# Kernel tuning notes

Hardware: AMD Instinct MI355X
Metric: run time of the kernel (lower is better)

## Reference

```python
import jax, jax.numpy as jnp
import numpy as np

SEQ_LEN = 4096
DIM_HALF = 2048  # x last dim = 2 * DIM_HALF
DIM_OUT = 1024
LN_EPS = 1e-5


def setup_inputs() -> dict:
    key = jax.random.key(0)
    k1, k2, k3 = jax.random.split(key, 3)
    x = jax.random.normal(k1, (SEQ_LEN, 2 * DIM_HALF), dtype=jnp.float32)
    ln_scale = jnp.ones((DIM_HALF,), dtype=jnp.float32)
    # original init is uniform(-eps/n, eps/n); scale randn similarly small
    spatial_weights = jax.random.normal(k2, (SEQ_LEN, SEQ_LEN), dtype=jnp.float32) * (0.001 / SEQ_LEN)
    spatial_biases = jnp.ones((SEQ_LEN, 1), dtype=jnp.float32)
    proj_w = jax.random.normal(k3, (DIM_HALF, DIM_OUT), dtype=jnp.float32) * (1.0 / np.sqrt(DIM_HALF))
    proj_b = jnp.zeros((DIM_OUT,), dtype=jnp.float32)
    return {"x": x, "ln_scale": ln_scale, "spatial_weights": spatial_weights,
            "spatial_biases": spatial_biases, "proj_w": proj_w, "proj_b": proj_b}


def reference(x, ln_scale, spatial_weights, spatial_biases, proj_w, proj_b):
    # split into value half and gate half
    xh, gate = jnp.split(x, 2, axis=-1)  # each (n, d)
    # LayerNorm (scale only, no offset), haiku default eps=1e-5
    mean = jnp.mean(gate, axis=-1, keepdims=True)
    var = jnp.var(gate, axis=-1, keepdims=True)
    gate = (gate - mean) * jax.lax.rsqrt(var + LN_EPS) * ln_scale
    # causal (lower-triangular) masked spatial mixing: out[m,d] = sum_n w[m,n] * gate[n,d]
    n = spatial_weights.shape[0]
    w = jnp.tril(spatial_weights)
    gate = jnp.einsum('nd,mn->md', gate, w) + spatial_biases  # (n, d)
    # gating multiply + output projection
    out = (xh * gate) @ proj_w + proj_b  # (n, dim_out)
    return out
```

## Files before the change

### kernel.cpp

```cpp
#include <hip/hip_runtime.h>
#include <cstdint>
#include <cstddef>

#define SEQ 4096
#define DH 2048
#define DOUT 1024

typedef float f32x4 __attribute__((ext_vector_type(4)));
typedef __bf16 bf16x8 __attribute__((ext_vector_type(8)));


__device__ __forceinline__ unsigned short f2bf(float f) {
  unsigned int u = __float_as_uint(f);
  unsigned int r = (u + 0x7FFFu + ((u >> 16) & 1u)) >> 16;
  return (unsigned short)r;
}

__device__ __forceinline__ void g2l16(const unsigned short* g, unsigned short* l) {
  __builtin_amdgcn_global_load_lds((__attribute__((address_space(1))) void*)(void*)g,
                                   (__attribute__((address_space(3))) void*)l, 16, 0, 0);
}


__global__ __launch_bounds__(256) void ln_stats(const float* __restrict__ x,
                                                float* __restrict__ mv,
                                                float* __restrict__ rv) {
  int row = blockIdx.x;
  const float4* g4 = (const float4*)(x + (size_t)row * (2 * DH) + DH);
  float4 a = g4[threadIdx.x];
  float4 b = g4[threadIdx.x + 256];
  float s  = a.x + a.y + a.z + a.w + b.x + b.y + b.z + b.w;
  float s2 = a.x * a.x + a.y * a.y + a.z * a.z + a.w * a.w +
             b.x * b.x + b.y * b.y + b.z * b.z + b.w * b.w;
#pragma unroll
  for (int o = 32; o > 0; o >>= 1) {
    s  += __shfl_down(s, o);
    s2 += __shfl_down(s2, o);
  }
  __shared__ float red[8];
  int wave = threadIdx.x >> 6;
  if ((threadIdx.x & 63) == 0) { red[wave] = s; red[wave + 4] = s2; }
  __syncthreads();
  if (threadIdx.x == 0) {
    float S  = red[0] + red[1] + red[2] + red[3];
    float S2 = red[4] + red[5] + red[6] + red[7];
    float mean = S * (1.0f / DH);
    float var  = S2 * (1.0f / DH) - mean * mean;
    mv[row] = mean;
    rv[row] = rsqrtf(var + 1e-5f);
  }
}


__global__ __launch_bounds__(256) void norm_tr(const float* __restrict__ x,
                                               const float* __restrict__ mv,
                                               const float* __restrict__ rv,
                                               const float* __restrict__ lns,
                                               unsigned short* __restrict__ gateT) {
  __shared__ float tile[64][65];
  int d0 = blockIdx.x * 64;
  int n0 = blockIdx.y * 64;
#pragma unroll
  for (int i = 0; i < 16; i++) {
    int idx = threadIdx.x + i * 256;
    int r = idx >> 6, c = idx & 63;
    float v = x[(size_t)(n0 + r) * (2 * DH) + DH + d0 + c];
    tile[r][c] = (v - mv[n0 + r]) * rv[n0 + r];
  }
  __syncthreads();
#pragma unroll
  for (int i = 0; i < 16; i++) {
    int idx = threadIdx.x + i * 256;
    int dr = idx >> 6, nc = idx & 63;
    float v = tile[nc][dr] * lns[d0 + dr];
    gateT[(size_t)(d0 + dr) * SEQ + n0 + nc] = f2bf(v);
  }
}


__global__ __launch_bounds__(256) void cast_w_tril(const float* __restrict__ w,
                                                   unsigned short* __restrict__ wb) {
  size_t e = ((size_t)blockIdx.x * 256 + threadIdx.x) * 8;
  int m = (int)(e >> 12);
  int k = (int)(e & 4095);
  uint4 o;
  if (k + 7 <= m) {
    const float4* s = (const float4*)(w + e);
    float4 a = s[0], b = s[1];
    o.x = (unsigned)f2bf(a.x) | ((unsigned)f2bf(a.y) << 16);
    o.y = (unsigned)f2bf(a.z) | ((unsigned)f2bf(a.w) << 16);
    o.z = (unsigned)f2bf(b.x) | ((unsigned)f2bf(b.y) << 16);
    o.w = (unsigned)f2bf(b.z) | ((unsigned)f2bf(b.w) << 16);
  } else if (k > m) {
    o.x = o.y = o.z = o.w = 0u;
  } else {
    unsigned short t[8];
#pragma unroll
    for (int j = 0; j < 8; j++) t[j] = (k + j <= m) ? f2bf(w[e + j]) : (unsigned short)0;
    o.x = (unsigned)t[0] | ((unsigned)t[1] << 16);
    o.y = (unsigned)t[2] | ((unsigned)t[3] << 16);
    o.z = (unsigned)t[4] | ((unsigned)t[5] << 16);
    o.w = (unsigned)t[6] | ((unsigned)t[7] << 16);
  }
  *(uint4*)(wb + e) = o;
}


__global__ __launch_bounds__(256) void proj_tr(const float* __restrict__ pw,
                                               unsigned short* __restrict__ pT) {
  __shared__ float tile[64][65];
  int j0 = blockIdx.x * 64;
  int d0 = blockIdx.y * 64;
#pragma unroll
  for (int i = 0; i < 16; i++) {
    int idx = threadIdx.x + i * 256;
    int r = idx >> 6, c = idx & 63;
    tile[r][c] = pw[(size_t)(d0 + r) * DOUT + j0 + c];
  }
  __syncthreads();
#pragma unroll
  for (int i = 0; i < 16; i++) {
    int idx = threadIdx.x + i * 256;
    int jr = idx >> 6, dc = idx & 63;
    pT[(size_t)(j0 + jr) * DH + d0 + dc] = f2bf(tile[dc][jr]);
  }
}


template <bool PAIR, int EPI>
__global__ __launch_bounds__(256) void gemm12864(const unsigned short* __restrict__ A,
                                                 const unsigned short* __restrict__ BT,
                                                 const float* __restrict__ xfull,
                                                 const float* __restrict__ rbias,
                                                 unsigned short* __restrict__ Pout,
                                                 const float* __restrict__ cbias,
                                                 float* __restrict__ out,
                                                 int N, int K) {
  constexpr int BK = 64;
  __shared__ unsigned short sA[128 * BK];
  __shared__ unsigned short sB[64 * BK];

  const int tid = threadIdx.x;
  const int lane = tid & 63, wave = tid >> 6;
  const int quad = lane >> 4, l16 = lane & 15;
  const int wm = wave >> 1, wn = wave & 1;
  const int bn0 = blockIdx.x * 64;
  const int p = blockIdx.y;

  int sOff[4], sDst[4];
#pragma unroll
  for (int r = 0; r < 4; r++) {
    int idx = r * 256 + tid;
    int row = idx >> 3;
    sOff[r] = row * K + (((idx & 7) ^ (row & 7)) * 8);
    sDst[r] = idx * 8;
  }

  const int nTiles = PAIR ? 2 : 1;
  for (int t = 0; t < nTiles; t++) {
    const int by = PAIR ? (t == 0 ? p : (2 * (int)gridDim.y - 1 - p)) : p;
    const int bm0 = by * 128;
    const int kEnd = PAIR ? (bm0 + 128) : K;

    const unsigned short* Ab = A + (size_t)bm0 * K;
    const unsigned short* Bb = BT + (size_t)bn0 * K;

    f32x4 acc[4][2] = {};

    for (int k0 = 0; k0 < kEnd; k0 += BK) {
#pragma unroll
      for (int r = 0; r < 4; r++) g2l16(Ab + k0 + sOff[r], &sA[sDst[r]]);
#pragma unroll
      for (int r = 0; r < 2; r++) g2l16(Bb + k0 + sOff[r], &sB[sDst[r]]);
      __syncthreads();

      bf16x8 af[2][4], bf[2][2];
#pragma unroll
      for (int h = 0; h < 2; h++) {
#pragma unroll
        for (int i = 0; i < 4; i++) {
          int R = wm * 64 + i * 16 + l16;
          af[h][i] = *(const bf16x8*)&sA[R * BK + (((h * 4 + quad) ^ (R & 7)) * 8)];
        }
#pragma unroll
        for (int j = 0; j < 2; j++) {
          int R = wn * 32 + j * 16 + l16;
          bf[h][j] = *(const bf16x8*)&sB[R * BK + (((h * 4 + quad) ^ (R & 7)) * 8)];
        }
      }
#pragma unroll
      for (int h = 0; h < 2; h++)
#pragma unroll
        for (int i = 0; i < 4; i++)
#pragma unroll
          for (int j = 0; j < 2; j++)
            acc[i][j] = __builtin_amdgcn_mfma_f32_16x16x32_bf16(af[h][i], bf[h][j], acc[i][j], 0, 0, 0);
      __syncthreads();
    }

#pragma unroll
    for (int i = 0; i < 4; i++) {
#pragma unroll
      for (int j = 0; j < 2; j++) {
        int col = bn0 + wn * 32 + j * 16 + l16;
#pragma unroll
        for (int r = 0; r < 4; r++) {
          int row = bm0 + wm * 64 + i * 16 + quad * 4 + r;
          float v = acc[i][j][r];
          if (EPI == 1) {
            float g = v + rbias[row];
            float pv = xfull[(size_t)row * (2 * DH) + col] * g;
            Pout[(size_t)row * N + col] = f2bf(pv);
          } else {
            out[(size_t)row * N + col] = v + cbias[col];
          }
        }
      }
    }
  }
}


extern "C" void kernel_launch(void* const* d_in, const int* in_sizes, int n_in,
                              void* d_out, int out_size, void* d_ws, size_t ws_size,
                              hipStream_t stream) {
  (void)in_sizes; (void)n_in; (void)out_size; (void)ws_size;
  const float* x   = (const float*)d_in[0];
  const float* lns = (const float*)d_in[1];
  const float* w   = (const float*)d_in[2];
  const float* sb  = (const float*)d_in[3];
  const float* pw  = (const float*)d_in[4];
  const float* pb  = (const float*)d_in[5];
  float* out = (float*)d_out;

  char* p = (char*)d_ws;
  unsigned short* gateT = (unsigned short*)p; p += (size_t)DH * SEQ * 2;
  unsigned short* wb    = (unsigned short*)p; p += (size_t)SEQ * SEQ * 2;
  unsigned short* projT = (unsigned short*)p; p += (size_t)DOUT * DH * 2;
  unsigned short* Pbuf  = (unsigned short*)p; p += (size_t)SEQ * DH * 2;
  float* mv = (float*)p; p += (size_t)SEQ * 4;
  float* rv = (float*)p; p += (size_t)SEQ * 4;

  ln_stats<<<SEQ, 256, 0, stream>>>(x, mv, rv);
  norm_tr<<<dim3(DH / 64, SEQ / 64), 256, 0, stream>>>(x, mv, rv, lns, gateT);
  cast_w_tril<<<(int)(((size_t)SEQ * SEQ / 8) / 256), 256, 0, stream>>>(w, wb);
  proj_tr<<<dim3(DOUT / 64, DH / 64), 256, 0, stream>>>(pw, projT);

  gemm12864<true, 1><<<dim3(DH / 64, SEQ / 256), 256, 0, stream>>>(
      wb, gateT, x, sb, Pbuf, nullptr, nullptr, DH, SEQ);
  gemm12864<false, 2><<<dim3(DOUT / 64, SEQ / 128), 256, 0, stream>>>(
      Pbuf, projT, nullptr, nullptr, nullptr, pb, out, DOUT, DH);
}
```

Measured before the change: 270.2 us.

## Double-buffer GEMM LDS tiles and cast only lower-triangular weight blocks

The GEMM kernel now keeps two LDS buffers and issues the global-to-LDS loads for the next K tile while MFMAs run on the current one. The paired causal tiles are fused into one continuous pipelined loop, with a mid-loop epilogue and accumulator reset. The weight cast kernel now launches one block per lower-triangular 128x128 tile and skips the strictly upper blocks entirely, cutting its read and write traffic roughly in half. This relies on the GEMM never reading upper-triangular blocks of wb (true, since kEnd=bm0+128), and it doubles LDS use per block, which may lower occupancy.

```diff
diff --git a/kernel.cpp b/kernel.cpp
--- a/kernel.cpp
+++ b/kernel.cpp
@@ -1,6 +1,7 @@
 #include <hip/hip_runtime.h>
 #include <cstdint>
 #include <cstddef>
+#include <math.h>
 
 #define SEQ 4096
 #define DH 2048
@@ -80,29 +81,40 @@
 
 __global__ __launch_bounds__(256) void cast_w_tril(const float* __restrict__ w,
                                                    unsigned short* __restrict__ wb) {
-  size_t e = ((size_t)blockIdx.x * 256 + threadIdx.x) * 8;
-  int m = (int)(e >> 12);
-  int k = (int)(e & 4095);
-  uint4 o;
-  if (k + 7 <= m) {
-    const float4* s = (const float4*)(w + e);
-    float4 a = s[0], b = s[1];
-    o.x = (unsigned)f2bf(a.x) | ((unsigned)f2bf(a.y) << 16);
-    o.y = (unsigned)f2bf(a.z) | ((unsigned)f2bf(a.w) << 16);
-    o.z = (unsigned)f2bf(b.x) | ((unsigned)f2bf(b.y) << 16);
-    o.w = (unsigned)f2bf(b.z) | ((unsigned)f2bf(b.w) << 16);
-  } else if (k > m) {
-    o.x = o.y = o.z = o.w = 0u;
-  } else {
-    unsigned short t[8];
-#pragma unroll
-    for (int j = 0; j < 8; j++) t[j] = (k + j <= m) ? f2bf(w[e + j]) : (unsigned short)0;
-    o.x = (unsigned)t[0] | ((unsigned)t[1] << 16);
-    o.y = (unsigned)t[2] | ((unsigned)t[3] << 16);
-    o.z = (unsigned)t[4] | ((unsigned)t[5] << 16);
-    o.w = (unsigned)t[6] | ((unsigned)t[7] << 16);
-  }
-  *(uint4*)(wb + e) = o;
+  int t = blockIdx.x;
+  int i0 = (int)((sqrtf(8.f * (float)t + 1.f) - 1.f) * 0.5f);
+  while ((i0 + 1) * (i0 + 2) / 2 <= t) i0++;
+  while (i0 * (i0 + 1) / 2 > t) i0--;
+  int j0 = t - i0 * (i0 + 1) / 2;
+  const bool interior = (j0 < i0);
+  const int rowBase = i0 * 128, colBase = j0 * 128;
+#pragma unroll
+  for (int rnd = 0; rnd < 8; rnd++) {
+    int idx = rnd * 256 + threadIdx.x;
+    int r = idx >> 4, g = idx & 15;
+    int m = rowBase + r, k = colBase + g * 8;
+    size_t e = (size_t)m * SEQ + k;
+    uint4 o;
+    if (interior || k + 7 <= m) {
+      const float4* s = (const float4*)(w + e);
+      float4 a = s[0], b = s[1];
+      o.x = (unsigned)f2bf(a.x) | ((unsigned)f2bf(a.y) << 16);
+      o.y = (unsigned)f2bf(a.z) | ((unsigned)f2bf(a.w) << 16);
+      o.z = (unsigned)f2bf(b.x) | ((unsigned)f2bf(b.y) << 16);
+      o.w = (unsigned)f2bf(b.z) | ((unsigned)f2bf(b.w) << 16);
+    } else if (k > m) {
+      o.x = o.y = o.z = o.w = 0u;
+    } else {
+      unsigned short tt[8];
+#pragma unroll
+      for (int j = 0; j < 8; j++) tt[j] = (k + j <= m) ? f2bf(w[e + j]) : (unsigned short)0;
+      o.x = (unsigned)tt[0] | ((unsigned)tt[1] << 16);
+      o.y = (unsigned)tt[2] | ((unsigned)tt[3] << 16);
+      o.z = (unsigned)tt[4] | ((unsigned)tt[5] << 16);
+      o.w = (unsigned)tt[6] | ((unsigned)tt[7] << 16);
+    }
+    *(uint4*)(wb + e) = o;
+  }
 }
 
 
@@ -128,17 +140,19 @@
 
 
 template <bool PAIR, int EPI>
-__global__ __launch_bounds__(256) void gemm12864(const unsigned short* __restrict__ A,
-                                                 const unsigned short* __restrict__ BT,
-                                                 const float* __restrict__ xfull,
-                                                 const float* __restrict__ rbias,
-                                                 unsigned short* __restrict__ Pout,
-                                                 const float* __restrict__ cbias,
-                                                 float* __restrict__ out,
-                                                 int N, int K) {
+__global__ __launch_bounds__(256) void gemm_db(const unsigned short* __restrict__ A,
+                                               const unsigned short* __restrict__ BT,
+                                               const float* __restrict__ xfull,
+                                               const float* __restrict__ rbias,
+                                               unsigned short* __restrict__ Pout,
+                                               const float* __restrict__ cbias,
+                                               float* __restrict__ out,
+                                               int N, int K) {
   constexpr int BK = 64;
-  __shared__ unsigned short sA[128 * BK];
-  __shared__ unsigned short sB[64 * BK];
+  __shared__ unsigned short sA0[128 * BK];
+  __shared__ unsigned short sA1[128 * BK];
+  __shared__ unsigned short sB0[64 * BK];
+  __shared__ unsigned short sB1[64 * BK];
 
   const int tid = threadIdx.x;
   const int lane = tid & 63, wave = tid >> 6;
@@ -147,6 +161,11 @@
   const int bn0 = blockIdx.x * 64;
   const int p = blockIdx.y;
 
+  const int bm0a = p * 128;
+  const int bm0b = PAIR ? (2 * (int)gridDim.y - 1 - p) * 128 : 0;
+  const int e1 = PAIR ? 2 * (p + 1) : 0x7fffffff;
+  const int total = PAIR ? (2 + 4 * (int)gridDim.y) : (K / BK);
+
   int sOff[4], sDst[4];
 #pragma unroll
   for (int r = 0; r < 4; r++) {
@@ -156,48 +175,45 @@
     sDst[r] = idx * 8;
   }
 
-  const int nTiles = PAIR ? 2 : 1;
-  for (int t = 0; t < nTiles; t++) {
-    const int by = PAIR ? (t == 0 ? p : (2 * (int)gridDim.y - 1 - p)) : p;
-    const int bm0 = by * 128;
-    const int kEnd = PAIR ? (bm0 + 128) : K;
-
-    const unsigned short* Ab = A + (size_t)bm0 * K;
-    const unsigned short* Bb = BT + (size_t)bn0 * K;
-
-    f32x4 acc[4][2] = {};
-
-    for (int k0 = 0; k0 < kEnd; k0 += BK) {
-#pragma unroll
-      for (int r = 0; r < 4; r++) g2l16(Ab + k0 + sOff[r], &sA[sDst[r]]);
-#pragma unroll
-      for (int r = 0; r < 2; r++) g2l16(Bb + k0 + sOff[r], &sB[sDst[r]]);
-      __syncthreads();
-
-      bf16x8 af[2][4], bf[2][2];
-#pragma unroll
-      for (int h = 0; h < 2; h++) {
-#pragma unroll
-        for (int i = 0; i < 4; i++) {
-          int R = wm * 64 + i * 16 + l16;
-          af[h][i] = *(const bf16x8*)&sA[R * BK + (((h * 4 + quad) ^ (R & 7)) * 8)];
-        }
-#pragma unroll
-        for (int j = 0; j < 2; j++) {
-          int R = wn * 32 + j * 16 + l16;
-          bf[h][j] = *(const bf16x8*)&sB[R * BK + (((h * 4 + quad) ^ (R & 7)) * 8)];
-        }
+  f32x4 acc[4][2] = {};
+
+  auto stage = [&](int i, unsigned short* dA, unsigned short* dB) {
+    int kk, bm;
+    if (!PAIR || i < e1) { kk = i * BK; bm = bm0a; }
+    else                 { kk = (i - e1) * BK; bm = bm0b; }
+    const unsigned short* Ab = A + (size_t)bm * K + kk;
+    const unsigned short* Bb = BT + (size_t)bn0 * K + kk;
+#pragma unroll
+    for (int r = 0; r < 4; r++) g2l16(Ab + sOff[r], dA + sDst[r]);
+#pragma unroll
+    for (int r = 0; r < 2; r++) g2l16(Bb + sOff[r], dB + sDst[r]);
+  };
+
+  auto compute = [&](const unsigned short* cA, const unsigned short* cB) {
+    bf16x8 af[2][4], bf[2][2];
+#pragma unroll
+    for (int h = 0; h < 2; h++) {
+#pragma unroll
+      for (int i = 0; i < 4; i++) {
+        int R = wm * 64 + i * 16 + l16;
+        af[h][i] = *(const bf16x8*)&cA[R * BK + (((h * 4 + quad) ^ (R & 7)) * 8)];
       }
 #pragma unroll
-      for (int h = 0; h < 2; h++)
-#pragma unroll
-        for (int i = 0; i < 4; i++)
-#pragma unroll
-          for (int j = 0; j < 2; j++)
-            acc[i][j] = __builtin_amdgcn_mfma_f32_16x16x32_bf16(af[h][i], bf[h][j], acc[i][j], 0, 0, 0);
-      __syncthreads();
-    }
-
+      for (int j = 0; j < 2; j++) {
+        int R = wn * 32 + j * 16 + l16;
+        bf[h][j] = *(const bf16x8*)&cB[R * BK + (((h * 4 + quad) ^ (R & 7)) * 8)];
+      }
+    }
+#pragma unroll
+    for (int h = 0; h < 2; h++)
+#pragma unroll
+      for (int i = 0; i < 4; i++)
+#pragma unroll
+        for (int j = 0; j < 2; j++)
+          acc[i][j] = __builtin_amdgcn_mfma_f32_16x16x32_bf16(af[h][i], bf[h][j], acc[i][j], 0, 0, 0);
+  };
+
+  auto epilogue = [&](int bm0) {
 #pragma unroll
     for (int i = 0; i < 4; i++) {
 #pragma unroll
@@ -217,7 +233,26 @@
         }
       }
     }
-  }
+  };
+
+  stage(0, sA0, sB0);
+  __syncthreads();
+  for (int i = 0; i < total; i += 2) {
+    stage(i + 1, sA1, sB1);
+    compute(sA0, sB0);
+    __syncthreads();
+    if (i + 2 < total) stage(i + 2, sA0, sB0);
+    compute(sA1, sB1);
+    if (PAIR && (i + 1) == e1 - 1) {
+      epilogue(bm0a);
+#pragma unroll
+      for (int a = 0; a < 4; a++)
+#pragma unroll
+        for (int b = 0; b < 2; b++) acc[a][b] = (f32x4){0.f, 0.f, 0.f, 0.f};
+    }
+    __syncthreads();
+  }
+  epilogue(PAIR ? bm0b : bm0a);
 }
 
 
@@ -243,11 +278,11 @@
 
   ln_stats<<<SEQ, 256, 0, stream>>>(x, mv, rv);
   norm_tr<<<dim3(DH / 64, SEQ / 64), 256, 0, stream>>>(x, mv, rv, lns, gateT);
-  cast_w_tril<<<(int)(((size_t)SEQ * SEQ / 8) / 256), 256, 0, stream>>>(w, wb);
+  cast_w_tril<<<528, 256, 0, stream>>>(w, wb);
   proj_tr<<<dim3(DOUT / 64, DH / 64), 256, 0, stream>>>(pw, projT);
 
-  gemm12864<true, 1><<<dim3(DH / 64, SEQ / 256), 256, 0, stream>>>(
+  gemm_db<true, 1><<<dim3(DH / 64, SEQ / 256), 256, 0, stream>>>(
       wb, gateT, x, sb, Pbuf, nullptr, nullptr, DH, SEQ);
-  gemm12864<false, 2><<<dim3(DOUT / 64, SEQ / 128), 256, 0, stream>>>(
+  gemm_db<false, 2><<<dim3(DOUT / 64, SEQ / 128), 256, 0, stream>>>(
       Pbuf, projT, nullptr, nullptr, nullptr, pb, out, DOUT, DH);
 }
```

Result: faster. 262.9 us (-2.7%).
